# Performance work log

Measured on AMD Instinct MI355X. Metric: run time of the kernel, lower is better.

The kernel has to match this reference:

```python
import jax, jax.numpy as jnp
import numpy as np

N, E, G = 20480, 163840, 512          # nodes, edges, graphs
D, H, R, L = 128, 4, 8, 4             # embed dim, heads, relations, layers
HK = H * D                            # heads * out_channels (RGATConv internal width)
BOARD_WIDTH = 7
NEG_SLOPE = 0.2                       # RGATConv leaky_relu slope


def setup_inputs() -> dict:
    key = jax.random.key(0)
    ks = jax.random.split(key, 12)
    s_in = 1.0 / np.sqrt(D)
    s_att = 1.0 / np.sqrt(HK)
    return {
        "x_nodes": jax.random.randint(ks[0], (N,), 0, 3),
        "edge_index": jax.random.randint(ks[1], (2, E), 0, N),
        "edge_type": jax.random.randint(ks[2], (E,), 0, R),
        "batch": jnp.arange(N) // (N // G),  # G graphs of N//G nodes each
        "emb": jax.random.normal(ks[3], (3, D), jnp.float32),
        "W": jax.random.normal(ks[4], (L, R, D, HK), jnp.float32) * s_in,
        "Q": jax.random.normal(ks[5], (L, HK, H), jnp.float32) * s_att,
        "K": jax.random.normal(ks[6], (L, HK, H), jnp.float32) * s_att,
        "B": jnp.zeros((L, D), jnp.float32),
        "fc1_w": jax.random.normal(ks[7], (D, 64), jnp.float32) * s_in,
        "fc1_b": jnp.zeros((64,), jnp.float32),
        "pol_w": jax.random.normal(ks[8], (64, BOARD_WIDTH), jnp.float32) * 0.125,
        "pol_b": jnp.zeros((BOARD_WIDTH,), jnp.float32),
        "val_w": jax.random.normal(ks[9], (64, 1), jnp.float32) * 0.125,
        "val_b": jnp.zeros((1,), jnp.float32),
    }


def _rgat_layer(x, W, Q, Km, b, src, dst, etype):
    # RGATConv, additive-self-attention, across-relation softmax, concat=False.
    x_all = jnp.einsum('nd,rdk->nrk', x, W)          # [N,R,HK] per-relation transform
    q_all = jnp.einsum('nrk,kh->nrh', x_all, Q)      # [N,R,H]
    k_all = jnp.einsum('nrk,kh->nrh', x_all, Km)     # [N,R,H]
    alpha = jax.nn.leaky_relu(q_all[dst, etype] + k_all[src, etype], NEG_SLOPE)  # [E,H]
    # segment softmax over destination nodes (across all relations)
    amax = jax.lax.stop_gradient(jax.ops.segment_max(alpha, dst, num_segments=N))
    ex = jnp.exp(alpha - amax[dst])
    denom = jax.ops.segment_sum(ex, dst, num_segments=N)
    a = ex / (denom[dst] + 1e-16)                    # [E,H]
    msg = x_all[src, etype].reshape(E, H, D) * a[:, :, None]   # [E,H,D]
    agg = jax.ops.segment_sum(msg.reshape(E, HK), dst, num_segments=N)
    out = agg.reshape(N, H, D).mean(axis=1) + b      # head-mean (concat=False) + bias
    return jax.nn.relu(out)


def reference(x_nodes, edge_index, edge_type, batch, emb, W, Q, K, B,
              fc1_w, fc1_b, pol_w, pol_b, val_w, val_b):
    src, dst = edge_index[0], edge_index[1]
    x = emb[x_nodes]                                  # [N,D]
    for l in range(L):
        x = _rgat_layer(x, W[l], Q[l], K[l], B[l], src, dst, edge_type)
    cnt = jax.ops.segment_sum(jnp.ones((N,), x.dtype), batch, num_segments=G)
    pooled = jax.ops.segment_sum(x, batch, num_segments=G) / jnp.maximum(cnt, 1.0)[:, None]
    h = jax.nn.relu(pooled @ fc1_w + fc1_b)           # [G,64]
    policy = h @ pol_w + pol_b                        # [G,BOARD_WIDTH]
    value = jnp.tanh(h @ val_w + val_b)               # [G,1]
    return policy, value
```

## Files before the change

kernel.cpp:

```cpp
#include <hip/hip_runtime.h>
#include <cstdint>
#include <cstddef>

constexpr int N_  = 20480;
constexpr int E_  = 163840;
constexpr int G_  = 512;
constexpr int D_  = 128;
constexpr int H_  = 4;
constexpr int R_  = 8;
constexpr int L_  = 4;
constexpr int HK_ = 512;
constexpr int NPG_ = N_ / G_;

typedef short short8 __attribute__((ext_vector_type(8)));
typedef float f32x4 __attribute__((ext_vector_type(4)));
typedef unsigned short u16;
typedef unsigned int u32;

__device__ inline u16 bfr(float f) {
  u32 u = __builtin_bit_cast(u32, f);
  return (u16)((u + 0x7fffu + ((u >> 16) & 1u)) >> 16);
}
__device__ inline float bf2f(u32 lo16) { return __builtin_bit_cast(float, lo16 << 16); }
__device__ inline float lrelu(float v) { return v >= 0.f ? v : 0.2f * v; }

__global__ void k_zero_i(int* __restrict__ p, int n) {
  int i = blockIdx.x * blockDim.x + threadIdx.x;
  if (i < n) p[i] = 0;
}

__global__ void k_count_rel(const int* __restrict__ dst, const int* __restrict__ et,
                            int* __restrict__ counts) {
  int e = blockIdx.x * blockDim.x + threadIdx.x;
  if (e < E_) atomicAdd(&counts[et[e] * N_ + dst[e]], 1);
}
__global__ void k_count_dst(const int* __restrict__ dst, int* __restrict__ counts) {
  int e = blockIdx.x * blockDim.x + threadIdx.x;
  if (e < E_) atomicAdd(&counts[dst[e]], 1);
}
__global__ void k_bsum(const int* __restrict__ c, int* __restrict__ bsum) {
  int t = threadIdx.x;
  const int4 v = *(const int4*)&c[blockIdx.x * 1024 + t * 4];
  int s = v.x + v.y + v.z + v.w;
#pragma unroll
  for (int o = 32; o; o >>= 1) s += __shfl_down(s, o, 64);
  __shared__ int ws_[4];
  if ((t & 63) == 0) ws_[t >> 6] = s;
  __syncthreads();
  if (t == 0) bsum[blockIdx.x] = ws_[0] + ws_[1] + ws_[2] + ws_[3];
}
__global__ void k_bscan(int* __restrict__ bsum, int nb, int* __restrict__ tot_out) {
  __shared__ int sh[512];
  int t = threadIdx.x;
  if (t < nb) sh[t] = bsum[t];
  __syncthreads();
  if (t == 0) {
    int run = 0;
    for (int i = 0; i < nb; ++i) { int v = sh[i]; sh[i] = run; run += v; }
    tot_out[0] = run;
  }
  __syncthreads();
  if (t < nb) bsum[t] = sh[t];
}
__global__ void k_scan3(const int* __restrict__ c, const int* __restrict__ bsum,
                        int* __restrict__ indptr, int* __restrict__ cursor) {
  __shared__ int ts[256];
  int t = threadIdx.x;
  int base = blockIdx.x * 1024 + t * 4;
  const int4 v = *(const int4*)&c[base];
  int s0 = v.x, s01 = v.x + v.y, s012 = s01 + v.z, s = s012 + v.w;
  ts[t] = s;
  __syncthreads();
#pragma unroll
  for (int o = 1; o < 256; o <<= 1) {
    int add = (t >= o) ? ts[t - o] : 0;
    __syncthreads();
    ts[t] += add;
    __syncthreads();
  }
  int off = bsum[blockIdx.x] + (t ? ts[t - 1] : 0);
  int4 o4 = make_int4(off, off + s0, off + s01, off + s012);
  *(int4*)&indptr[base] = o4;
  *(int4*)&cursor[base] = o4;
}
__global__ void k_scatter_rel(const int* __restrict__ dst, const int* __restrict__ et,
                              const int* __restrict__ src, int* __restrict__ cursor,
                              int* __restrict__ esort, int* __restrict__ slotOf,
                              int* __restrict__ srcR) {
  int e = blockIdx.x * blockDim.x + threadIdx.x;
  if (e < E_) {
    int p = atomicAdd(&cursor[et[e] * N_ + dst[e]], 1);
    esort[p] = e;
    slotOf[e] = p;
    srcR[p] = src[e];
  }
}
__global__ void k_scatter_dst(const int* __restrict__ dst, int* __restrict__ cursor,
                              int* __restrict__ esort) {
  int e = blockIdx.x * blockDim.x + threadIdx.x;
  if (e < E_) {
    int p = atomicAdd(&cursor[dst[e]], 1);
    esort[p] = e;
  }
}
__global__ void k_padbase(const int* __restrict__ indptrR, int* __restrict__ padBase) {
  if (threadIdx.x == 0 && blockIdx.x == 0) {
    int cum = 0;
    for (int r = 0; r < R_; ++r) {
      padBase[r] = cum;
      int cnt = indptrR[(r + 1) * N_] - indptrR[r * N_];
      cum += (cnt + 127) & ~127;
    }
    padBase[R_] = cum;
  }
}

__global__ void k_embed(const int* __restrict__ xn, const float* __restrict__ emb,
                        float* __restrict__ x, u16* __restrict__ xb) {
  int i = blockIdx.x * blockDim.x + threadIdx.x;
  if (i < N_ * D_) {
    int n = i >> 7, d = i & 127;
    float v = emb[xn[n] * D_ + d];
    x[i] = v;
    xb[i] = bfr(v);
  }
}

__global__ __launch_bounds__(256) void k_wqk_all(const float* __restrict__ W,
                                                 const float* __restrict__ Q,
                                                 const float* __restrict__ Km,
                                                 float* __restrict__ WQK) {
  int gw = (blockIdx.x * 256 + threadIdx.x) >> 6;
  int lane = threadIdx.x & 63;
  int d = gw & 127, r = (gw >> 7) & 7, l = gw >> 10;
  const float* wrow = W + (((size_t)l * R_ + r) * D_ + d) * HK_;
  const float* Ql = Q + (size_t)l * HK_ * H_;
  const float* Kl = Km + (size_t)l * HK_ * H_;
  float acc[8] = {0.f, 0.f, 0.f, 0.f, 0.f, 0.f, 0.f, 0.f};
#pragma unroll
  for (int it = 0; it < 8; ++it) {
    int k = it * 64 + lane;
    float w = wrow[k];
    const float4 qv = *(const float4*)&Ql[k * 4];
    const float4 kv = *(const float4*)&Kl[k * 4];
    acc[0] += w * qv.x; acc[1] += w * qv.y; acc[2] += w * qv.z; acc[3] += w * qv.w;
    acc[4] += w * kv.x; acc[5] += w * kv.y; acc[6] += w * kv.z; acc[7] += w * kv.w;
  }
#pragma unroll
  for (int o = 32; o; o >>= 1)
#pragma unroll
    for (int j = 0; j < 8; ++j) acc[j] += __shfl_down(acc[j], o, 64);
  if (lane == 0) {
#pragma unroll
    for (int h = 0; h < 4; ++h) {
      WQK[((size_t)l * D_ + d) * 64 + r * 4 + h] = acc[h];
      WQK[((size_t)l * D_ + d) * 64 + 32 + r * 4 + h] = acc[4 + h];
    }
  }
}

__global__ __launch_bounds__(256) void k_qk(const float* __restrict__ x,
                                            const float* __restrict__ WQK,
                                            float* __restrict__ q,
                                            float* __restrict__ kk) {
  __shared__ float xs[32][129];
  __shared__ float wq[128][64];
  const int t = threadIdx.x;
  const int n0 = blockIdx.x * 32;
#pragma unroll
  for (int p = 0; p < 4; ++p) {
    int idx = t + p * 256;
    int row = idx >> 5, c4 = (idx & 31) * 4;
    const float4 v = *(const float4*)&x[(size_t)(n0 + row) * D_ + c4];
    xs[row][c4 + 0] = v.x; xs[row][c4 + 1] = v.y;
    xs[row][c4 + 2] = v.z; xs[row][c4 + 3] = v.w;
  }
#pragma unroll
  for (int p = 0; p < 8; ++p) {
    int idx = t + p * 256;
    int row = idx >> 4, c4 = (idx & 15) * 4;
    *(float4*)&wq[row][c4] = *(const float4*)&WQK[row * 64 + c4];
  }
  __syncthreads();
  const int node = t >> 3, cq = t & 7;
  float s[8];
#pragma unroll
  for (int j = 0; j < 8; ++j) s[j] = 0.f;
  for (int k = 0; k < 128; ++k) {
    float xv = xs[node][k];
#pragma unroll
    for (int j = 0; j < 8; ++j) s[j] = fmaf(xv, wq[k][cq * 8 + j], s[j]);
  }
#pragma unroll
  for (int j = 0; j < 8; ++j) {
    int c = cq * 8 + j;
    if (c < 32) q[(size_t)(n0 + node) * 32 + c] = s[j];
    else        kk[(size_t)(n0 + node) * 32 + (c - 32)] = s[j];
  }
}

__global__ __launch_bounds__(256) void k_attn(
    const int* __restrict__ ipN, const int* __restrict__ esD,
    const int* __restrict__ src, const int* __restrict__ et,
    const float* __restrict__ q, const float* __restrict__ kk,
    const int* __restrict__ slotOf, float* __restrict__ aw) {
  int n = blockIdx.x * 4 + (threadIdx.x >> 6);
  int lane = threadIdx.x & 63;
  int j0 = ipN[n], j1 = ipN[n + 1];
  int deg = j1 - j0;
  if (deg == 0) return;
  int h = lane & 3;
  if (deg <= 16) {
    int ei = lane >> 2;
    float a = -3.4e38f;
    int slot = 0;
    if (ei < deg) {
      int e = esD[j0 + ei];
      int r = et[e];
      slot = slotOf[e];
      a = lrelu(q[(size_t)n * 32 + r * 4 + h] + kk[(size_t)src[e] * 32 + r * 4 + h]);
    }
    float m = a;
#pragma unroll
    for (int o = 4; o < 64; o <<= 1) m = fmaxf(m, __shfl_xor(m, o, 64));
    float ex = (ei < deg) ? expf(a - m) : 0.f;
    float s = ex;
#pragma unroll
    for (int o = 4; o < 64; o <<= 1) s += __shfl_xor(s, o, 64);
    if (ei < deg) aw[(size_t)slot * 4 + h] = ex * (0.25f / (s + 1e-16f));
    return;
  }
  int nch = (deg + 15) >> 4;
  float m = -3.4e38f;
  for (int c = 0; c < nch; ++c) {
    int ei = c * 16 + (lane >> 2);
    if (ei < deg) {
      int e = esD[j0 + ei];
      int r = et[e];
      float a = lrelu(q[(size_t)n * 32 + r * 4 + h] + kk[(size_t)src[e] * 32 + r * 4 + h]);
      m = fmaxf(m, a);
    }
  }
#pragma unroll
  for (int o = 4; o < 64; o <<= 1) m = fmaxf(m, __shfl_xor(m, o, 64));
  float s = 0.f;
  for (int c = 0; c < nch; ++c) {
    int ei = c * 16 + (lane >> 2);
    if (ei < deg) {
      int e = esD[j0 + ei];
      int r = et[e];
      float a = lrelu(q[(size_t)n * 32 + r * 4 + h] + kk[(size_t)src[e] * 32 + r * 4 + h]);
      float ex = expf(a - m);
      s += ex;
      aw[(size_t)slotOf[e] * 4 + h] = ex;
    }
  }
#pragma unroll
  for (int o = 4; o < 64; o <<= 1) s += __shfl_xor(s, o, 64);
  float inv = 0.25f / (s + 1e-16f);
  for (int c = 0; c < nch; ++c) {
    int ei = c * 16 + (lane >> 2);
    if (ei < deg) {
      int e = esD[j0 + ei];
      aw[(size_t)slotOf[e] * 4 + h] *= inv;
    }
  }
}

__global__ void k_cvt_w_all(const float* __restrict__ W, u16* __restrict__ wt) {
  __shared__ u16 tile[64][65];
  const int z = blockIdx.z, k0 = blockIdx.y * 64, c0 = blockIdx.x * 64;
  const int t = threadIdx.x;
  const int tk = t >> 4, tc4 = (t & 15) * 4;
  const float* Wz = W + (size_t)z * D_ * HK_;
  u16* wz = wt + (size_t)z * HK_ * D_;
#pragma unroll
  for (int p = 0; p < 4; ++p) {
    int krow = tk + p * 16;
    const float4 v = *(const float4*)&Wz[(size_t)(k0 + krow) * HK_ + c0 + tc4];
    tile[tc4 + 0][krow] = bfr(v.x);
    tile[tc4 + 1][krow] = bfr(v.y);
    tile[tc4 + 2][krow] = bfr(v.z);
    tile[tc4 + 3][krow] = bfr(v.w);
  }
  __syncthreads();
#pragma unroll
  for (int p = 0; p < 4; ++p) {
    int crow = tk + p * 16;
    uint2 o;
    o.x = (u32)tile[crow][tc4 + 0] | ((u32)tile[crow][tc4 + 1] << 16);
    o.y = (u32)tile[crow][tc4 + 2] | ((u32)tile[crow][tc4 + 3] << 16);
    *(uint2*)&wz[(size_t)(c0 + crow) * D_ + k0 + tc4] = o;
  }
}

__global__ __launch_bounds__(512, 1) void k_edge7(
    const u16* __restrict__ xb, const u16* __restrict__ wt,
    const int* __restrict__ indptrR, const int* __restrict__ padBase,
    const int* __restrict__ srcR, const float* __restrict__ aw,
    u16* __restrict__ m) {
  __shared__ u16 atile[128 * 128];
  __shared__ float awl[128][4];
  __shared__ int srcl[128];
  const int t = threadIdx.x;
  const int b128 = blockIdx.x * 128;
  if (b128 >= padBase[R_]) return;
  int r = 0;
  while (b128 >= padBase[r + 1]) ++r;
  const int ip0 = indptrR[r * N_];
  const int cnt = indptrR[(r + 1) * N_] - ip0;
  const int local0 = b128 - padBase[r];
  const u16* wrp = wt + (size_t)r * HK_ * D_;
  const int wid = t >> 6, lane = t & 63;
  const int l15 = lane & 15, l4 = lane >> 4;
  short8 breg[4][4];
#pragma unroll
  for (int ks = 0; ks < 4; ++ks)
#pragma unroll
    for (int h = 0; h < 4; ++h) {
      int c = (wid + 8 * h) * 16 + l15;
      breg[ks][h] = *(const short8*)(wrp + (size_t)c * 128 + ks * 32 + l4 * 8);
    }
  if (t < 128) {
    int lidx = local0 + t;
    if (lidx < cnt) {
      srcl[t] = srcR[ip0 + lidx];
      *(float4*)awl[t] = *(const float4*)(aw + (size_t)(ip0 + lidx) * 4);
    } else {
      srcl[t] = 0;
      *(float4*)awl[t] = make_float4(0.f, 0.f, 0.f, 0.f);
    }
  }
  __syncthreads();
#pragma unroll
  for (int p = 0; p < 4; ++p) {
    int idx = t + p * 512;
    int row = idx >> 4, seg = idx & 15;
    uint4 v = *(const uint4*)(xb + (size_t)srcl[row] * 128 + seg * 8);
    *(uint4*)((char*)atile + row * 256 + ((seg * 16) ^ ((row & 7) << 4))) = v;
  }
  __syncthreads();
  f32x4 acc[8][4];
#pragma unroll
  for (int i = 0; i < 8; ++i)
#pragma unroll
    for (int h = 0; h < 4; ++h) acc[i][h] = (f32x4){0.f, 0.f, 0.f, 0.f};
#pragma unroll
  for (int ks = 0; ks < 4; ++ks) {
    short8 av[8];
#pragma unroll
    for (int i = 0; i < 8; ++i) {
      int row = i * 16 + l15;
      av[i] = *(const short8*)((char*)atile + row * 256 +
                ((l4 * 16 + ks * 64) ^ ((row & 7) << 4)));
    }
#pragma unroll
    for (int i = 0; i < 8; ++i)
#pragma unroll
      for (int h = 0; h < 4; ++h)
        acc[i][h] = __builtin_amdgcn_mfma_f32_16x16x32_bf16(breg[ks][h], av[i],
                                                            acc[i][h], 0, 0, 0);
  }
  __syncthreads();
#pragma unroll
  for (int i = 0; i < 8; ++i) {
    int row = i * 16 + l15;
    const float4 awf = *(const float4*)awl[row];
    float v0 = awf.x * acc[i][0][0] + awf.y * acc[i][1][0] + awf.z * acc[i][2][0] + awf.w * acc[i][3][0];
    float v1 = awf.x * acc[i][0][1] + awf.y * acc[i][1][1] + awf.z * acc[i][2][1] + awf.w * acc[i][3][1];
    float v2 = awf.x * acc[i][0][2] + awf.y * acc[i][1][2] + awf.z * acc[i][2][2] + awf.w * acc[i][3][2];
    float v3 = awf.x * acc[i][0][3] + awf.y * acc[i][1][3] + awf.z * acc[i][2][3] + awf.w * acc[i][3][3];
    uint2 o;
    o.x = (u32)bfr(v0) | ((u32)bfr(v1) << 16);
    o.y = (u32)bfr(v2) | ((u32)bfr(v3) << 16);
    *(uint2*)((char*)atile + row * 256 + ((wid * 32 + l4 * 8) ^ ((row & 7) << 4))) = o;
  }
  __syncthreads();
  {
    int row = t >> 2, c0 = (t & 3) * 64;
    char* gout = (char*)(m + (size_t)(b128 + row) * 128) + c0;
#pragma unroll
    for (int qq = 0; qq < 4; ++qq) {
      uint4 v = *(const uint4*)((char*)atile + row * 256 + ((c0 + qq * 16) ^ ((row & 7) << 4)));
      *(uint4*)(gout + qq * 16) = v;
    }
  }
}

__global__ __launch_bounds__(256) void k_aggqk(
    const int* __restrict__ indptrR, const int* __restrict__ padBase,
    const u16* __restrict__ m, const float* __restrict__ Bl,
    const float* __restrict__ WQK, int doqk,
    float* __restrict__ xout, u16* __restrict__ xbout,
    float* __restrict__ q, float* __restrict__ kk) {
  __shared__ float wqs[128 * 64];
  __shared__ float xrow[4][128];
  const int t = threadIdx.x;
  if (doqk) {
#pragma unroll
    for (int p = 0; p < 8; ++p)
      *(float4*)&wqs[(t + p * 256) * 4] = *(const float4*)&WQK[(t + p * 256) * 4];
  }
  const int w = t >> 6;
  int n = blockIdx.x * 4 + w;
  int lane = t & 63;
  float s0 = 0.f, s1 = 0.f;
#pragma unroll
  for (int r = 0; r < R_; ++r) {
    int ip0 = indptrR[r * N_];
    int j0 = indptrR[r * N_ + n], j1 = indptrR[r * N_ + n + 1];
    int base = padBase[r] + (j0 - ip0);
    int cntn = j1 - j0;
    int j = 0;
    for (; j + 1 < cntn; j += 2) {
      u32 v0 = *((const u32*)(m + (size_t)(base + j) * 128) + lane);
      u32 v1 = *((const u32*)(m + (size_t)(base + j + 1) * 128) + lane);
      s0 += bf2f(v0 & 0xffffu) + bf2f(v1 & 0xffffu);
      s1 += bf2f(v0 >> 16) + bf2f(v1 >> 16);
    }
    if (j < cntn) {
      u32 v0 = *((const u32*)(m + (size_t)(base + j) * 128) + lane);
      s0 += bf2f(v0 & 0xffffu);
      s1 += bf2f(v0 >> 16);
    }
  }
  float2 o;
  o.x = fmaxf(s0 + Bl[2 * lane], 0.f);
  o.y = fmaxf(s1 + Bl[2 * lane + 1], 0.f);
  *((float2*)(xout + (size_t)n * D_) + lane) = o;
  ((u32*)(xbout + (size_t)n * D_))[lane] = (u32)bfr(o.x) | ((u32)bfr(o.y) << 16);
  if (doqk) {
    xrow[w][2 * lane] = o.x;
    xrow[w][2 * lane + 1] = o.y;
    __syncthreads();
    const float* xr = xrow[w];
    float s = 0.f;
#pragma unroll
    for (int d4 = 0; d4 < 32; ++d4) {
      const float4 xv = *(const float4*)&xr[d4 * 4];
      s += xv.x * wqs[(d4 * 4 + 0) * 64 + lane] + xv.y * wqs[(d4 * 4 + 1) * 64 + lane] +
           xv.z * wqs[(d4 * 4 + 2) * 64 + lane] + xv.w * wqs[(d4 * 4 + 3) * 64 + lane];
    }
    if (lane < 32) q[(size_t)n * 32 + lane] = s;
    else           kk[(size_t)n * 32 + (lane - 32)] = s;
  }
}

__global__ void k_pool(const float* __restrict__ x, float* __restrict__ pooled) {
  int i = blockIdx.x * blockDim.x + threadIdx.x;
  if (i >= G_ * D_) return;
  int d = i & 127, g = i >> 7;
  float s = 0.f;
  for (int j = 0; j < NPG_; ++j) s += x[(size_t)(g * NPG_ + j) * D_ + d];
  pooled[i] = s * (1.0f / NPG_);
}

__global__ void k_head(const float* __restrict__ pooled, const float* __restrict__ fc1w,
                       const float* __restrict__ fc1b, const float* __restrict__ polw,
                       const float* __restrict__ polb, const float* __restrict__ valw,
                       const float* __restrict__ valb, float* __restrict__ out) {
  int g = blockIdx.x;
  int t = threadIdx.x;
  __shared__ float hb[64];
  const float* p = pooled + (size_t)g * D_;
  float s = fc1b[t];
  for (int d = 0; d < D_; ++d) s += p[d] * fc1w[d * 64 + t];
  hb[t] = fmaxf(s, 0.f);
  __syncthreads();
  if (t < 7) {
    float s2 = polb[t];
    for (int j = 0; j < 64; ++j) s2 += hb[j] * polw[j * 7 + t];
    out[g * 7 + t] = s2;
  } else if (t == 7) {
    float s2 = valb[0];
    for (int j = 0; j < 64; ++j) s2 += hb[j] * valw[j];
    out[G_ * 7 + g] = tanhf(s2);
  }
}

extern "C" void kernel_launch(void* const* d_in, const int* in_sizes, int n_in,
                              void* d_out, int out_size, void* d_ws, size_t ws_size,
                              hipStream_t stream) {
  (void)in_sizes; (void)n_in; (void)out_size;
  const int*   x_nodes = (const int*)d_in[0];
  const int*   eidx    = (const int*)d_in[1];
  const int*   etype   = (const int*)d_in[2];
  const float* emb     = (const float*)d_in[4];
  const float* W       = (const float*)d_in[5];
  const float* Q       = (const float*)d_in[6];
  const float* Km      = (const float*)d_in[7];
  const float* B       = (const float*)d_in[8];
  const float* fc1w    = (const float*)d_in[9];
  const float* fc1b    = (const float*)d_in[10];
  const float* polw    = (const float*)d_in[11];
  const float* polb    = (const float*)d_in[12];
  const float* valw    = (const float*)d_in[13];
  const float* valb    = (const float*)d_in[14];
  float* out = (float*)d_out;
  const int* srcA = eidx;
  const int* dstA = eidx + E_;

  char* p = (char*)d_ws;
  size_t used = 0;
  auto carve = [&](size_t bytes) {
    char* q = p;
    size_t adv = (bytes + 255) & ~(size_t)255;
    p += adv;
    used += adv;
    return q;
  };
  float* x_cur  = (float*)carve((size_t)N_ * D_ * 4);
  float* x_nxt  = (float*)carve((size_t)N_ * D_ * 4);
  u16*   xbf    = (u16*)carve((size_t)N_ * D_ * 2);
  u16*   mbuf   = (u16*)carve((size_t)(E_ + R_ * 128) * D_ * 2);
  float* qbuf   = (float*)carve((size_t)N_ * 32 * 4);
  float* kbuf   = (float*)carve((size_t)N_ * 32 * 4);
  float* awbuf  = (float*)carve((size_t)E_ * H_ * 4);
  float* WQKb   = (float*)carve((size_t)L_ * D_ * 64 * 4);
  u16*   Wtb    = (u16*)carve((size_t)L_ * R_ * HK_ * D_ * 2);
  float* pooled = (float*)carve((size_t)G_ * D_ * 4);
  int* countsR  = (int*)carve((size_t)R_ * N_ * 4);
  int* cursorR  = (int*)carve((size_t)R_ * N_ * 4);
  int* indptrR  = (int*)carve((size_t)(R_ * N_ + 1) * 4);
  int* esortR   = (int*)carve((size_t)E_ * 4);
  int* slotOf   = (int*)carve((size_t)E_ * 4);
  int* srcR     = (int*)carve((size_t)E_ * 4);
  int* countsN  = (int*)carve((size_t)N_ * 4);
  int* cursorN  = (int*)carve((size_t)N_ * 4);
  int* indptrN  = (int*)carve((size_t)(N_ + 1) * 4);
  int* esortD   = (int*)carve((size_t)E_ * 4);
  int* padBase  = (int*)carve((size_t)(R_ + 1) * 4);
  int* bsum     = (int*)carve((size_t)512 * 4);
  if (used > ws_size) return;

  constexpr int RN = R_ * N_;
  constexpr int NBR = RN / 1024;
  constexpr int NBN = N_ / 1024;
  constexpr int EDGE_BLOCKS = E_ / 128 + R_;

  k_zero_i<<<(RN + 255) / 256, 256, 0, stream>>>(countsR, RN);
  k_zero_i<<<(N_ + 255) / 256, 256, 0, stream>>>(countsN, N_);
  k_count_rel<<<E_ / 256, 256, 0, stream>>>(dstA, etype, countsR);
  k_count_dst<<<E_ / 256, 256, 0, stream>>>(dstA, countsN);
  k_bsum<<<NBR, 256, 0, stream>>>(countsR, bsum);
  k_bscan<<<1, 512, 0, stream>>>(bsum, NBR, indptrR + RN);
  k_scan3<<<NBR, 256, 0, stream>>>(countsR, bsum, indptrR, cursorR);
  k_scatter_rel<<<E_ / 256, 256, 0, stream>>>(dstA, etype, srcA, cursorR, esortR,
                                              slotOf, srcR);
  k_bsum<<<NBN, 256, 0, stream>>>(countsN, bsum);
  k_bscan<<<1, 512, 0, stream>>>(bsum, NBN, indptrN + N_);
  k_scan3<<<NBN, 256, 0, stream>>>(countsN, bsum, indptrN, cursorN);
  k_scatter_dst<<<E_ / 256, 256, 0, stream>>>(dstA, cursorN, esortD);
  k_padbase<<<1, 64, 0, stream>>>(indptrR, padBase);
  k_embed<<<(N_ * D_) / 256, 256, 0, stream>>>(x_nodes, emb, x_cur, xbf);
  k_wqk_all<<<(L_ * R_ * D_ * 64) / 256, 256, 0, stream>>>(W, Q, Km, WQKb);
  k_cvt_w_all<<<dim3(HK_ / 64, D_ / 64, L_ * R_), 256, 0, stream>>>(W, Wtb);
  k_qk<<<N_ / 32, 256, 0, stream>>>(x_cur, WQKb, qbuf, kbuf);

  for (int l = 0; l < L_; ++l) {
    const float* Bl = B + (size_t)l * D_;
    k_attn<<<N_ / 4, 256, 0, stream>>>(indptrN, esortD, srcA, etype, qbuf, kbuf,
                                       slotOf, awbuf);
    k_edge7<<<EDGE_BLOCKS, 512, 0, stream>>>(xbf, Wtb + (size_t)l * R_ * HK_ * D_,
                                             indptrR, padBase, srcR, awbuf, mbuf);
    int doqk = (l < L_ - 1) ? 1 : 0;
    k_aggqk<<<N_ / 4, 256, 0, stream>>>(indptrR, padBase, mbuf, Bl,
                                        WQKb + (size_t)(l + 1) * D_ * 64 * (doqk ? 1 : 0),
                                        doqk, x_nxt, xbf, qbuf, kbuf);
    float* tmp = x_cur; x_cur = x_nxt; x_nxt = tmp;
  }

  k_pool<<<(G_ * D_) / 256, 256, 0, stream>>>(x_cur, pooled);
  k_head<<<G_, 64, 0, stream>>>(pooled, fc1w, fc1b, polw, polb, valw, valb, out);
}
```

Measured before the change: 532.7 us.

## Fuse CSR build kernels, fold embedding into qk, separate edge output buffer

Merges the paired relation/destination CSR preprocessing kernels (zero, count, block-sum, scan, scatter) into single launches, computes padBase inside the block-scan, and folds the embedding lookup into the initial q/k projection kernel. This cuts roughly nine kernel launches and drops the unused esortR writes. The edge GEMM kernel gains a separate shared output tile so the barrier before the epilogue can be removed, at the cost of 32KB more LDS per block.

```diff
diff --git a/kernel.cpp b/kernel.cpp
--- a/kernel.cpp
+++ b/kernel.cpp
@@ -24,49 +24,85 @@
 __device__ inline float bf2f(u32 lo16) { return __builtin_bit_cast(float, lo16 << 16); }
 __device__ inline float lrelu(float v) { return v >= 0.f ? v : 0.2f * v; }
 
-__global__ void k_zero_i(int* __restrict__ p, int n) {
+__global__ void k_zero2(int* __restrict__ cR, int* __restrict__ cN) {
   int i = blockIdx.x * blockDim.x + threadIdx.x;
-  if (i < n) p[i] = 0;
-}
-
-__global__ void k_count_rel(const int* __restrict__ dst, const int* __restrict__ et,
-                            int* __restrict__ counts) {
+  if (i < R_ * N_) cR[i] = 0;
+  else if (i < R_ * N_ + N_) cN[i - R_ * N_] = 0;
+}
+
+__global__ void k_count_both(const int* __restrict__ dst, const int* __restrict__ et,
+                             int* __restrict__ cR, int* __restrict__ cN) {
   int e = blockIdx.x * blockDim.x + threadIdx.x;
-  if (e < E_) atomicAdd(&counts[et[e] * N_ + dst[e]], 1);
-}
-__global__ void k_count_dst(const int* __restrict__ dst, int* __restrict__ counts) {
-  int e = blockIdx.x * blockDim.x + threadIdx.x;
-  if (e < E_) atomicAdd(&counts[dst[e]], 1);
-}
-__global__ void k_bsum(const int* __restrict__ c, int* __restrict__ bsum) {
+  if (e < E_) {
+    int d = dst[e];
+    atomicAdd(&cR[et[e] * N_ + d], 1);
+    atomicAdd(&cN[d], 1);
+  }
+}
+
+__global__ void k_bsum2(const int* __restrict__ cR, const int* __restrict__ cN,
+                        int* __restrict__ bsumR, int* __restrict__ bsumN) {
+  int b = blockIdx.x;
+  const int* src = (b < 160) ? &cR[b * 1024] : &cN[(b - 160) * 1024];
   int t = threadIdx.x;
-  const int4 v = *(const int4*)&c[blockIdx.x * 1024 + t * 4];
+  const int4 v = *(const int4*)&src[t * 4];
   int s = v.x + v.y + v.z + v.w;
 #pragma unroll
   for (int o = 32; o; o >>= 1) s += __shfl_down(s, o, 64);
   __shared__ int ws_[4];
   if ((t & 63) == 0) ws_[t >> 6] = s;
   __syncthreads();
-  if (t == 0) bsum[blockIdx.x] = ws_[0] + ws_[1] + ws_[2] + ws_[3];
-}
-__global__ void k_bscan(int* __restrict__ bsum, int nb, int* __restrict__ tot_out) {
-  __shared__ int sh[512];
+  if (t == 0) {
+    int tot = ws_[0] + ws_[1] + ws_[2] + ws_[3];
+    if (b < 160) bsumR[b] = tot; else bsumN[b - 160] = tot;
+  }
+}
+
+__global__ void k_bscan2(int* __restrict__ bsumR, int* __restrict__ bsumN,
+                         int* __restrict__ totR, int* __restrict__ totN,
+                         int* __restrict__ padBase) {
+  __shared__ int shR[160];
+  __shared__ int shN[20];
   int t = threadIdx.x;
-  if (t < nb) sh[t] = bsum[t];
+  if (t < 160) shR[t] = bsumR[t];
+  if (t < 20) shN[t] = bsumN[t];
   __syncthreads();
   if (t == 0) {
     int run = 0;
-    for (int i = 0; i < nb; ++i) { int v = sh[i]; sh[i] = run; run += v; }
-    tot_out[0] = run;
-  }
-  __syncthreads();
-  if (t < nb) bsum[t] = sh[t];
-}
-__global__ void k_scan3(const int* __restrict__ c, const int* __restrict__ bsum,
-                        int* __restrict__ indptr, int* __restrict__ cursor) {
+    for (int i = 0; i < 160; ++i) { int v = shR[i]; shR[i] = run; run += v; }
+    totR[0] = run;
+    int cum = 0;
+    for (int r = 0; r < R_; ++r) {
+      padBase[r] = cum;
+      int lo = shR[r * 20];
+      int hi = (r == R_ - 1) ? run : shR[(r + 1) * 20];
+      cum += (hi - lo + 127) & ~127;
+    }
+    padBase[R_] = cum;
+    int run2 = 0;
+    for (int i = 0; i < 20; ++i) { int v = shN[i]; shN[i] = run2; run2 += v; }
+    totN[0] = run2;
+  }
+  __syncthreads();
+  if (t < 160) bsumR[t] = shR[t];
+  if (t < 20) bsumN[t] = shN[t];
+}
+
+__global__ void k_scan32(const int* __restrict__ cR, const int* __restrict__ cN,
+                         const int* __restrict__ bsumR, const int* __restrict__ bsumN,
+                         int* __restrict__ ipR, int* __restrict__ curR,
+                         int* __restrict__ ipN, int* __restrict__ curN) {
   __shared__ int ts[256];
+  int b = blockIdx.x;
+  const int* c;
+  int off0;
+  int* indptr;
+  int* cursor;
+  int lb;
+  if (b < 160) { c = cR; off0 = bsumR[b]; indptr = ipR; cursor = curR; lb = b; }
+  else { c = cN; off0 = bsumN[b - 160]; indptr = ipN; cursor = curN; lb = b - 160; }
   int t = threadIdx.x;
-  int base = blockIdx.x * 1024 + t * 4;
+  int base = lb * 1024 + t * 4;
   const int4 v = *(const int4*)&c[base];
   int s0 = v.x, s01 = v.x + v.y, s012 = s01 + v.z, s = s012 + v.w;
   ts[t] = s;
@@ -78,51 +114,24 @@
     ts[t] += add;
     __syncthreads();
   }
-  int off = bsum[blockIdx.x] + (t ? ts[t - 1] : 0);
+  int off = off0 + (t ? ts[t - 1] : 0);
   int4 o4 = make_int4(off, off + s0, off + s01, off + s012);
   *(int4*)&indptr[base] = o4;
   *(int4*)&cursor[base] = o4;
 }
-__global__ void k_scatter_rel(const int* __restrict__ dst, const int* __restrict__ et,
-                              const int* __restrict__ src, int* __restrict__ cursor,
-                              int* __restrict__ esort, int* __restrict__ slotOf,
-                              int* __restrict__ srcR) {
+
+__global__ void k_scatter_both(const int* __restrict__ dst, const int* __restrict__ et,
+                               const int* __restrict__ src, int* __restrict__ curR,
+                               int* __restrict__ curN, int* __restrict__ slotOf,
+                               int* __restrict__ srcR, int* __restrict__ esortD) {
   int e = blockIdx.x * blockDim.x + threadIdx.x;
   if (e < E_) {
-    int p = atomicAdd(&cursor[et[e] * N_ + dst[e]], 1);
-    esort[p] = e;
+    int d = dst[e];
+    int p = atomicAdd(&curR[et[e] * N_ + d], 1);
     slotOf[e] = p;
     srcR[p] = src[e];
-  }
-}
-__global__ void k_scatter_dst(const int* __restrict__ dst, int* __restrict__ cursor,
-                              int* __restrict__ esort) {
-  int e = blockIdx.x * blockDim.x + threadIdx.x;
-  if (e < E_) {
-    int p = atomicAdd(&cursor[dst[e]], 1);
-    esort[p] = e;
-  }
-}
-__global__ void k_padbase(const int* __restrict__ indptrR, int* __restrict__ padBase) {
-  if (threadIdx.x == 0 && blockIdx.x == 0) {
-    int cum = 0;
-    for (int r = 0; r < R_; ++r) {
-      padBase[r] = cum;
-      int cnt = indptrR[(r + 1) * N_] - indptrR[r * N_];
-      cum += (cnt + 127) & ~127;
-    }
-    padBase[R_] = cum;
-  }
-}
-
-__global__ void k_embed(const int* __restrict__ xn, const float* __restrict__ emb,
-                        float* __restrict__ x, u16* __restrict__ xb) {
-  int i = blockIdx.x * blockDim.x + threadIdx.x;
-  if (i < N_ * D_) {
-    int n = i >> 7, d = i & 127;
-    float v = emb[xn[n] * D_ + d];
-    x[i] = v;
-    xb[i] = bfr(v);
+    int p2 = atomicAdd(&curN[d], 1);
+    esortD[p2] = e;
   }
 }
 
@@ -159,27 +168,31 @@
   }
 }
 
-__global__ __launch_bounds__(256) void k_qk(const float* __restrict__ x,
-                                            const float* __restrict__ WQK,
-                                            float* __restrict__ q,
-                                            float* __restrict__ kk) {
+__global__ __launch_bounds__(256) void k_embed_qk(
+    const int* __restrict__ xn, const float* __restrict__ emb,
+    const float* __restrict__ WQK, float* __restrict__ x, u16* __restrict__ xb,
+    float* __restrict__ q, float* __restrict__ kk) {
   __shared__ float xs[32][129];
   __shared__ float wq[128][64];
+  __shared__ int xnl[32];
   const int t = threadIdx.x;
   const int n0 = blockIdx.x * 32;
-#pragma unroll
-  for (int p = 0; p < 4; ++p) {
-    int idx = t + p * 256;
-    int row = idx >> 5, c4 = (idx & 31) * 4;
-    const float4 v = *(const float4*)&x[(size_t)(n0 + row) * D_ + c4];
-    xs[row][c4 + 0] = v.x; xs[row][c4 + 1] = v.y;
-    xs[row][c4 + 2] = v.z; xs[row][c4 + 3] = v.w;
-  }
+  if (t < 32) xnl[t] = xn[n0 + t];
 #pragma unroll
   for (int p = 0; p < 8; ++p) {
     int idx = t + p * 256;
     int row = idx >> 4, c4 = (idx & 15) * 4;
     *(float4*)&wq[row][c4] = *(const float4*)&WQK[row * 64 + c4];
+  }
+  __syncthreads();
+#pragma unroll
+  for (int p = 0; p < 16; ++p) {
+    int idx = t + p * 256;
+    int node = idx >> 7, d = idx & 127;
+    float v = emb[xnl[node] * D_ + d];
+    xs[node][d] = v;
+    x[(size_t)(n0 + node) * D_ + d] = v;
+    xb[(size_t)(n0 + node) * D_ + d] = bfr(v);
   }
   __syncthreads();
   const int node = t >> 3, cq = t & 7;
@@ -294,12 +307,13 @@
   }
 }
 
-__global__ __launch_bounds__(512, 1) void k_edge7(
+__global__ __launch_bounds__(512, 1) void k_edge8(
     const u16* __restrict__ xb, const u16* __restrict__ wt,
     const int* __restrict__ indptrR, const int* __restrict__ padBase,
     const int* __restrict__ srcR, const float* __restrict__ aw,
     u16* __restrict__ m) {
   __shared__ u16 atile[128 * 128];
+  __shared__ u16 outb[128 * 128];
   __shared__ float awl[128][4];
   __shared__ int srcl[128];
   const int t = threadIdx.x;
@@ -361,7 +375,6 @@
         acc[i][h] = __builtin_amdgcn_mfma_f32_16x16x32_bf16(breg[ks][h], av[i],
                                                             acc[i][h], 0, 0, 0);
   }
-  __syncthreads();
 #pragma unroll
   for (int i = 0; i < 8; ++i) {
     int row = i * 16 + l15;
@@ -373,7 +386,7 @@
     uint2 o;
     o.x = (u32)bfr(v0) | ((u32)bfr(v1) << 16);
     o.y = (u32)bfr(v2) | ((u32)bfr(v3) << 16);
-    *(uint2*)((char*)atile + row * 256 + ((wid * 32 + l4 * 8) ^ ((row & 7) << 4))) = o;
+    *(uint2*)((char*)outb + row * 256 + ((wid * 32 + l4 * 8) ^ ((row & 7) << 4))) = o;
   }
   __syncthreads();
   {
@@ -381,7 +394,7 @@
     char* gout = (char*)(m + (size_t)(b128 + row) * 128) + c0;
 #pragma unroll
     for (int qq = 0; qq < 4; ++qq) {
-      uint4 v = *(const uint4*)((char*)atile + row * 256 + ((c0 + qq * 16) ^ ((row & 7) << 4)));
+      uint4 v = *(const uint4*)((char*)outb + row * 256 + ((c0 + qq * 16) ^ ((row & 7) << 4)));
       *(uint4*)(gout + qq * 16) = v;
     }
   }
@@ -522,7 +535,6 @@
   int* countsR  = (int*)carve((size_t)R_ * N_ * 4);
   int* cursorR  = (int*)carve((size_t)R_ * N_ * 4);
   int* indptrR  = (int*)carve((size_t)(R_ * N_ + 1) * 4);
-  int* esortR   = (int*)carve((size_t)E_ * 4);
   int* slotOf   = (int*)carve((size_t)E_ * 4);
   int* srcR     = (int*)carve((size_t)E_ * 4);
   int* countsN  = (int*)carve((size_t)N_ * 4);
@@ -530,38 +542,30 @@
   int* indptrN  = (int*)carve((size_t)(N_ + 1) * 4);
   int* esortD   = (int*)carve((size_t)E_ * 4);
   int* padBase  = (int*)carve((size_t)(R_ + 1) * 4);
-  int* bsum     = (int*)carve((size_t)512 * 4);
+  int* bsumR    = (int*)carve((size_t)160 * 4);
+  int* bsumN    = (int*)carve((size_t)32 * 4);
   if (used > ws_size) return;
 
   constexpr int RN = R_ * N_;
-  constexpr int NBR = RN / 1024;
-  constexpr int NBN = N_ / 1024;
   constexpr int EDGE_BLOCKS = E_ / 128 + R_;
 
-  k_zero_i<<<(RN + 255) / 256, 256, 0, stream>>>(countsR, RN);
-  k_zero_i<<<(N_ + 255) / 256, 256, 0, stream>>>(countsN, N_);
-  k_count_rel<<<E_ / 256, 256, 0, stream>>>(dstA, etype, countsR);
-  k_count_dst<<<E_ / 256, 256, 0, stream>>>(dstA, countsN);
-  k_bsum<<<NBR, 256, 0, stream>>>(countsR, bsum);
-  k_bscan<<<1, 512, 0, stream>>>(bsum, NBR, indptrR + RN);
-  k_scan3<<<NBR, 256, 0, stream>>>(countsR, bsum, indptrR, cursorR);
-  k_scatter_rel<<<E_ / 256, 256, 0, stream>>>(dstA, etype, srcA, cursorR, esortR,
-                                              slotOf, srcR);
-  k_bsum<<<NBN, 256, 0, stream>>>(countsN, bsum);
-  k_bscan<<<1, 512, 0, stream>>>(bsum, NBN, indptrN + N_);
-  k_scan3<<<NBN, 256, 0, stream>>>(countsN, bsum, indptrN, cursorN);
-  k_scatter_dst<<<E_ / 256, 256, 0, stream>>>(dstA, cursorN, esortD);
-  k_padbase<<<1, 64, 0, stream>>>(indptrR, padBase);
-  k_embed<<<(N_ * D_) / 256, 256, 0, stream>>>(x_nodes, emb, x_cur, xbf);
+  k_zero2<<<(RN + N_ + 255) / 256, 256, 0, stream>>>(countsR, countsN);
+  k_count_both<<<E_ / 256, 256, 0, stream>>>(dstA, etype, countsR, countsN);
+  k_bsum2<<<180, 256, 0, stream>>>(countsR, countsN, bsumR, bsumN);
+  k_bscan2<<<1, 256, 0, stream>>>(bsumR, bsumN, indptrR + RN, indptrN + N_, padBase);
+  k_scan32<<<180, 256, 0, stream>>>(countsR, countsN, bsumR, bsumN,
+                                    indptrR, cursorR, indptrN, cursorN);
+  k_scatter_both<<<E_ / 256, 256, 0, stream>>>(dstA, etype, srcA, cursorR, cursorN,
+                                               slotOf, srcR, esortD);
   k_wqk_all<<<(L_ * R_ * D_ * 64) / 256, 256, 0, stream>>>(W, Q, Km, WQKb);
   k_cvt_w_all<<<dim3(HK_ / 64, D_ / 64, L_ * R_), 256, 0, stream>>>(W, Wtb);
-  k_qk<<<N_ / 32, 256, 0, stream>>>(x_cur, WQKb, qbuf, kbuf);
+  k_embed_qk<<<N_ / 32, 256, 0, stream>>>(x_nodes, emb, WQKb, x_cur, xbf, qbuf, kbuf);
 
   for (int l = 0; l < L_; ++l) {
     const float* Bl = B + (size_t)l * D_;
     k_attn<<<N_ / 4, 256, 0, stream>>>(indptrN, esortD, srcA, etype, qbuf, kbuf,
                                        slotOf, awbuf);
-    k_edge7<<<EDGE_BLOCKS, 512, 0, stream>>>(xbf, Wtb + (size_t)l * R_ * HK_ * D_,
+    k_edge8<<<EDGE_BLOCKS, 512, 0, stream>>>(xbf, Wtb + (size_t)l * R_ * HK_ * D_,
                                              indptrR, padBase, srcR, awbuf, mbuf);
     int doqk = (l < L_ - 1) ? 1 : 0;
     k_aggqk<<<N_ / 4, 256, 0, stream>>>(indptrR, padBase, mbuf, Bl,
```

Result: faster. 502.3 us, median of 2 (-5.7%).
